# Performance work log

Hardware: AMD Instinct MI355X
Metric: run time of the kernel (lower is better)

## Reference

```python
import jax, jax.numpy as jnp
import numpy as np

D = 512      # d_encoder
H = 8        # num_attn_heads
DH = 64      # d_attn
B = 8
S = 1024


def setup_inputs() -> dict:
    key = jax.random.key(0)
    ks = jax.random.split(key, 12)
    lim_in = 1.0 / np.sqrt(D)
    inp = {
        "Q": jax.random.normal(ks[0], (B, S, D), dtype=jnp.float32),
        "K": jax.random.normal(ks[1], (B, S, D), dtype=jnp.float32),
        "V": jax.random.normal(ks[2], (B, S, D), dtype=jnp.float32),
        # per-head projection weights stacked over heads: [H, D, DH]
        "Wq": jax.random.uniform(ks[3], (H, D, DH), jnp.float32, -lim_in, lim_in),
        "bq": jax.random.uniform(ks[4], (H, DH), jnp.float32, -lim_in, lim_in),
        "Wk": jax.random.uniform(ks[5], (H, D, DH), jnp.float32, -lim_in, lim_in),
        "bk": jax.random.uniform(ks[6], (H, DH), jnp.float32, -lim_in, lim_in),
        "Wv": jax.random.uniform(ks[7], (H, D, DH), jnp.float32, -lim_in, lim_in),
        "bv": jax.random.uniform(ks[8], (H, DH), jnp.float32, -lim_in, lim_in),
        "Wo": jax.random.uniform(ks[9], (D, D), jnp.float32, -lim_in, lim_in),
        "bo": jax.random.uniform(ks[10], (D,), jnp.float32, -lim_in, lim_in),
    }
    return inp


def reference(Q, K, V, Wq, bq, Wk, bk, Wv, bv, Wo, bo):
    scale = 1.0 / np.sqrt(DH).astype(np.float32)
    # per-head projections (the torch loop over heads, batched): [B,H,S,DH]
    Qh = jnp.einsum("bsd,hde->bhse", Q, Wq) + bq[None, :, None, :]
    Kh = jnp.einsum("bsd,hde->bhse", K, Wk) + bk[None, :, None, :]
    Vh = jnp.einsum("bsd,hde->bhse", V, Wv) + bv[None, :, None, :]
    # scaled dot-product attention with materialized scores [B,H,S,S]
    scores = jnp.einsum("bhse,bhte->bhst", Qh, Kh) * scale
    probs = jax.nn.softmax(scores, axis=-1)
    x = jnp.einsum("bhst,bhte->bhse", probs, Vh)  # [B,H,S,DH]
    # NOTE: original torch code does x.view(B, S, H*DH) directly on the
    # (B,H,S,DH) contiguous tensor WITHOUT transposing heads/time; we
    # faithfully replicate that memory-layout reshape.
    x = x.reshape(B, S, H * DH)
    x = x @ Wo + bo
    # dropout p=0.0 (p_drop set to 0 for deterministic reference)
    return x
```

## Files before the change

kernel.cpp:

```cpp
#include <hip/hip_runtime.h>
#include <hip/hip_bf16.h>

#define D_ENC 512
#define NH 8
#define DHD 64
#define BB 8
#define SS 1024

typedef unsigned short u16;
typedef __attribute__((ext_vector_type(8))) short short8;
typedef __attribute__((ext_vector_type(4))) float floatx4;

#define QSCALE 0.18033688011112042f

__device__ inline u16 f2bf(float f) {
    __hip_bfloat16 h = __float2bfloat16(f);
    return *reinterpret_cast<u16*>(&h);
}

__device__ inline void glds16(const u16* g, u16* l) {
    __builtin_amdgcn_global_load_lds(
        (const __attribute__((address_space(1))) void*)g,
        (__attribute__((address_space(3))) void*)l, 16, 0, 0);
}

__global__ __launch_bounds__(256) void prep_all(
    const float* __restrict__ Wq, const float* __restrict__ Wk,
    const float* __restrict__ Wv, const float* __restrict__ Wo,
    const float* __restrict__ Q, const float* __restrict__ K,
    const float* __restrict__ V,
    u16* __restrict__ WqT, u16* __restrict__ WkT, u16* __restrict__ WvT,
    u16* __restrict__ WoT, u16* __restrict__ Xbf)
{
    int bx = blockIdx.x;
    if (bx < 4096) {
        int tid = bx * 256 + threadIdx.x;
        const int WSZ = NH * D_ENC * DHD;
        if (tid < 3 * WSZ) {
            int wi = tid / WSZ, r = tid % WSZ;
            int d = r & 511;
            int e = (r >> 9) & 63;
            int h = r >> 15;
            const float* src = wi == 0 ? Wq : (wi == 1 ? Wk : Wv);
            u16* dst = wi == 0 ? WqT : (wi == 1 ? WkT : WvT);
            dst[r] = f2bf(src[h * (D_ENC * DHD) + d * DHD + e]);
        } else {
            int r = tid - 3 * WSZ;
            int d = r & 511, n = r >> 9;
            WoT[r] = f2bf(Wo[d * D_ENC + n]);
        }
    } else {
        int t = (bx - 4096) * 256 + threadIdx.x;
        int p = t / 524288, i = t % 524288;
        const float* src = p == 0 ? Q : (p == 1 ? K : V);
        const float4* s4 = reinterpret_cast<const float4*>(src) + (size_t)i * 2;
        float4 a = s4[0], b = s4[1];
        u16 hv[8] = { f2bf(a.x), f2bf(a.y), f2bf(a.z), f2bf(a.w),
                      f2bf(b.x), f2bf(b.y), f2bf(b.z), f2bf(b.w) };
        *reinterpret_cast<uint4*>(Xbf + (size_t)t * 8) =
            *reinterpret_cast<const uint4*>(hv);
    }
}

__global__ __launch_bounds__(256, 4) void qkv_gemm(
    const u16* __restrict__ Xbf,
    const u16* __restrict__ WqT, const u16* __restrict__ WkT,
    const u16* __restrict__ WvT,
    const float* __restrict__ bq, const float* __restrict__ bk,
    const float* __restrict__ bv,
    u16* __restrict__ Qh, u16* __restrict__ Kh, u16* __restrict__ VhT)
{
    const int proj = blockIdx.z;
    const u16* X = Xbf + (size_t)proj * (BB * SS * D_ENC);
    const u16* WT = proj == 0 ? WqT : (proj == 1 ? WkT : WvT);
    const float* bias = proj == 0 ? bq : (proj == 1 ? bk : bv);
    u16* out = proj == 0 ? Qh : (proj == 1 ? Kh : VhT);
    const float oscale = proj == 0 ? QSCALE : 1.0f;

    const int m0 = blockIdx.x * 128;
    const int n0 = blockIdx.y * 64;
    __shared__ __align__(16) char smem[(128 * 64 + 64 * 64) * 2];
    u16* As = (u16*)smem;
    u16* Bs = As + 128 * 64;
    u16* Ts = (u16*)smem;

    const int tid = threadIdx.x, lane = tid & 63, w = tid >> 6;
    const int q = lane >> 4, l15 = lane & 15;
    const int lr = lane >> 3;
    const int lc = (lane & 7) ^ (lr & 7);

    floatx4 acc[2][4] = {};

    for (int d0 = 0; d0 < D_ENC; d0 += 64) {
        #pragma unroll
        for (int j = 0; j < 4; ++j) {
            int r = (j * 4 + w) * 8 + lr;
            glds16(X + (size_t)(m0 + r) * D_ENC + d0 + lc * 8,
                   As + (j * 4 + w) * 512);
        }
        #pragma unroll
        for (int j = 0; j < 2; ++j) {
            int r = (j * 4 + w) * 8 + lr;
            glds16(WT + (size_t)(n0 + r) * D_ENC + d0 + lc * 8,
                   Bs + (j * 4 + w) * 512);
        }
        __syncthreads();
        #pragma unroll
        for (int ks = 0; ks < 2; ++ks) {
            const int co = ((ks * 4 + q) ^ (l15 & 7)) * 8;
            short8 a0 = *(const short8*)&As[(32 * w + l15) * 64 + co];
            short8 a1 = *(const short8*)&As[(32 * w + 16 + l15) * 64 + co];
            #pragma unroll
            for (int f = 0; f < 4; ++f) {
                short8 bf = *(const short8*)&Bs[(f * 16 + l15) * 64 + co];
                acc[0][f] = __builtin_amdgcn_mfma_f32_16x16x32_bf16(a0, bf, acc[0][f], 0, 0, 0);
                acc[1][f] = __builtin_amdgcn_mfma_f32_16x16x32_bf16(a1, bf, acc[1][f], 0, 0, 0);
            }
        }
        __syncthreads();
    }

    const int b = m0 >> 10, sb = m0 & 1023, h = n0 >> 6;
    if (proj < 2) {
        u16* dst = out + ((size_t)(b * NH + h) * SS + sb) * DHD;
        #pragma unroll
        for (int i = 0; i < 2; ++i)
            #pragma unroll
            for (int f = 0; f < 4; ++f) {
                float bv_ = bias[n0 + f * 16 + l15];
                #pragma unroll
                for (int r = 0; r < 4; ++r)
                    dst[(32 * w + 16 * i + q * 4 + r) * DHD + f * 16 + l15] =
                        f2bf((acc[i][f][r] + bv_) * oscale);
            }
    } else {
        #pragma unroll
        for (int i = 0; i < 2; ++i)
            #pragma unroll
            for (int f = 0; f < 4; ++f) {
                float bv_ = bias[n0 + f * 16 + l15];
                #pragma unroll
                for (int r = 0; r < 4; ++r)
                    Ts[(f * 16 + l15) * 136 + 32 * w + 16 * i + q * 4 + r] =
                        f2bf(acc[i][f][r] + bv_);
            }
        __syncthreads();
        u16* dst = out + (size_t)(b * NH + h) * DHD * SS + sb;
        #pragma unroll
        for (int p2 = 0; p2 < 4; ++p2) {
            int c = (tid + 256 * p2) * 8;
            int e = c >> 7, s = c & 127;
            uint4 v = *(const uint4*)&Ts[e * 136 + s];
            *(uint4*)&dst[(size_t)e * SS + s] = v;
        }
    }
}

__global__ __launch_bounds__(256, 4) void flash_attn(
    const u16* __restrict__ Qh, const u16* __restrict__ Kh,
    const u16* __restrict__ VhT, u16* __restrict__ Xb)
{
    const int i = blockIdx.x;
    const int s0 = (i >> 6) * 64;
    const int bh_i = ((i >> 3) & 7) * 8 + (i & 7);
    const size_t bh = (size_t)bh_i;

    __shared__ __align__(16) u16 Ks[2][64 * 64], Vs[2][64 * 64], Ps[64 * 64];

    const int tid = threadIdx.x, lane = tid & 63, w = tid >> 6;
    const int q = lane >> 4, l15 = lane & 15;
    const int lr = lane >> 3, lc = (lane & 7) ^ (lr & 7);

    const u16* qrow = Qh + (bh * SS + s0 + 16 * w + l15) * DHD;
    short8 qb0 = *(const short8*)(qrow + q * 8);
    short8 qb1 = *(const short8*)(qrow + 32 + q * 8);

    const u16* kbase = Kh + bh * SS * DHD;
    const u16* vbase = VhT + bh * DHD * SS;

    #pragma unroll
    for (int j = 0; j < 2; ++j) {
        int r = (j * 4 + w) * 8 + lr;
        glds16(kbase + (size_t)r * DHD + lc * 8, Ks[0] + (j * 4 + w) * 512);
        glds16(vbase + (size_t)r * SS + lc * 8, Vs[0] + (j * 4 + w) * 512);
    }

    floatx4 O[4] = {};
    floatx4 L = {0.f, 0.f, 0.f, 0.f};
    const short8 ones = {16256, 16256, 16256, 16256,
                         16256, 16256, 16256, 16256};

    for (int kt = 0; kt < SS / 64; ++kt) {
        __syncthreads();
        if (kt + 1 < SS / 64) {
            const int k1 = (kt + 1) * 64;
            u16* kd = Ks[(kt + 1) & 1];
            u16* vd = Vs[(kt + 1) & 1];
            #pragma unroll
            for (int j = 0; j < 2; ++j) {
                int r = (j * 4 + w) * 8 + lr;
                glds16(kbase + (size_t)(k1 + r) * DHD + lc * 8,
                       kd + (j * 4 + w) * 512);
                glds16(vbase + (size_t)r * SS + k1 + lc * 8,
                       vd + (j * 4 + w) * 512);
            }
        }
        const u16* ks_ = Ks[kt & 1];
        const u16* vs_ = Vs[kt & 1];

        floatx4 sacc[4] = {};
        #pragma unroll
        for (int f = 0; f < 4; ++f) {
            const int co0 = (q ^ (l15 & 7)) * 8;
            const int co1 = ((4 + q) ^ (l15 & 7)) * 8;
            short8 ka0 = *(const short8*)&ks_[(f * 16 + l15) * 64 + co0];
            short8 ka1 = *(const short8*)&ks_[(f * 16 + l15) * 64 + co1];
            sacc[f] = __builtin_amdgcn_mfma_f32_16x16x32_bf16(ka0, qb0, sacc[f], 0, 0, 0);
            sacc[f] = __builtin_amdgcn_mfma_f32_16x16x32_bf16(ka1, qb1, sacc[f], 0, 0, 0);
        }

        #pragma unroll
        for (int f = 0; f < 4; ++f) {
            ushort4 pk;
            pk.x = f2bf(__builtin_amdgcn_exp2f(sacc[f][0]));
            pk.y = f2bf(__builtin_amdgcn_exp2f(sacc[f][1]));
            pk.z = f2bf(__builtin_amdgcn_exp2f(sacc[f][2]));
            pk.w = f2bf(__builtin_amdgcn_exp2f(sacc[f][3]));
            const int chunk = (2 * f + (q >> 1)) ^ (l15 & 7);
            *(ushort4*)&Ps[(16 * w + l15) * 64 + chunk * 8 + (q & 1) * 4] = pk;
        }

        #pragma unroll
        for (int ks = 0; ks < 2; ++ks) {
            const int co = ((ks * 4 + q) ^ (l15 & 7)) * 8;
            short8 pa = *(const short8*)&Ps[(16 * w + l15) * 64 + co];
            L = __builtin_amdgcn_mfma_f32_16x16x32_bf16(pa, ones, L, 0, 0, 0);
            #pragma unroll
            for (int f = 0; f < 4; ++f) {
                short8 vb = *(const short8*)&vs_[(f * 16 + l15) * 64 + co];
                O[f] = __builtin_amdgcn_mfma_f32_16x16x32_bf16(pa, vb, O[f], 0, 0, 0);
            }
        }
    }

    u16* dst = Xb + (bh * SS + s0) * DHD;
    #pragma unroll
    for (int f = 0; f < 4; ++f)
        #pragma unroll
        for (int r = 0; r < 4; ++r)
            dst[(16 * w + q * 4 + r) * DHD + f * 16 + l15] =
                f2bf(O[f][r] / L[r]);
}

__global__ __launch_bounds__(256, 4) void out_gemm(
    const u16* __restrict__ X, const u16* __restrict__ WT,
    const float* __restrict__ bias, float* __restrict__ out)
{
    const int m0 = blockIdx.x * 128;
    const int n0 = blockIdx.y * 64;
    __shared__ __align__(16) u16 As[128 * 64];
    __shared__ __align__(16) u16 Bs[64 * 64];

    const int tid = threadIdx.x, lane = tid & 63, w = tid >> 6;
    const int q = lane >> 4, l15 = lane & 15;
    const int lr = lane >> 3, lc = (lane & 7) ^ (lr & 7);

    floatx4 acc[2][4] = {};

    for (int d0 = 0; d0 < D_ENC; d0 += 64) {
        #pragma unroll
        for (int j = 0; j < 4; ++j) {
            int r = (j * 4 + w) * 8 + lr;
            glds16(X + (size_t)(m0 + r) * D_ENC + d0 + lc * 8,
                   As + (j * 4 + w) * 512);
        }
        #pragma unroll
        for (int j = 0; j < 2; ++j) {
            int r = (j * 4 + w) * 8 + lr;
            glds16(WT + (size_t)(n0 + r) * D_ENC + d0 + lc * 8,
                   Bs + (j * 4 + w) * 512);
        }
        __syncthreads();
        #pragma unroll
        for (int ks = 0; ks < 2; ++ks) {
            const int co = ((ks * 4 + q) ^ (l15 & 7)) * 8;
            short8 a0 = *(const short8*)&As[(32 * w + l15) * 64 + co];
            short8 a1 = *(const short8*)&As[(32 * w + 16 + l15) * 64 + co];
            #pragma unroll
            for (int f = 0; f < 4; ++f) {
                short8 bf = *(const short8*)&Bs[(f * 16 + l15) * 64 + co];
                acc[0][f] = __builtin_amdgcn_mfma_f32_16x16x32_bf16(a0, bf, acc[0][f], 0, 0, 0);
                acc[1][f] = __builtin_amdgcn_mfma_f32_16x16x32_bf16(a1, bf, acc[1][f], 0, 0, 0);
            }
        }
        __syncthreads();
    }
    #pragma unroll
    for (int i = 0; i < 2; ++i)
        #pragma unroll
        for (int f = 0; f < 4; ++f) {
            float bv_ = bias[n0 + f * 16 + l15];
            #pragma unroll
            for (int r = 0; r < 4; ++r)
                out[(size_t)(m0 + 32 * w + 16 * i + q * 4 + r) * D_ENC +
                    n0 + f * 16 + l15] = acc[i][f][r] + bv_;
        }
}

extern "C" void kernel_launch(void* const* d_in, const int* in_sizes, int n_in,
                              void* d_out, int out_size, void* d_ws, size_t ws_size,
                              hipStream_t stream)
{
    const float* Q  = (const float*)d_in[0];
    const float* K  = (const float*)d_in[1];
    const float* V  = (const float*)d_in[2];
    const float* Wq = (const float*)d_in[3];
    const float* bq = (const float*)d_in[4];
    const float* Wk = (const float*)d_in[5];
    const float* bk = (const float*)d_in[6];
    const float* Wv = (const float*)d_in[7];
    const float* bv = (const float*)d_in[8];
    const float* Wo = (const float*)d_in[9];
    const float* bo = (const float*)d_in[10];
    float* out = (float*)d_out;

    char* ws = (char*)d_ws;
    u16* WqT = (u16*)(ws + 0);
    u16* WkT = (u16*)(ws + 524288);
    u16* WvT = (u16*)(ws + 1048576);
    u16* WoT = (u16*)(ws + 1572864);
    u16* Xbf = (u16*)(ws + 2097152);
    u16* Xb  = (u16*)(ws + 2097152);
    u16* Qh  = (u16*)(ws + 27262976);
    u16* Kh  = (u16*)(ws + 35651584);
    u16* VhT = (u16*)(ws + 44040192);

    hipLaunchKernelGGL(prep_all, dim3(10240), dim3(256), 0, stream,
                       Wq, Wk, Wv, Wo, Q, K, V, WqT, WkT, WvT, WoT, Xbf);
    hipLaunchKernelGGL(qkv_gemm, dim3(64, 8, 3), dim3(256), 0, stream,
                       Xbf, WqT, WkT, WvT, bq, bk, bv, Qh, Kh, VhT);
    hipLaunchKernelGGL(flash_attn, dim3(1024), dim3(256), 0, stream,
                       Qh, Kh, VhT, Xb);
    hipLaunchKernelGGL(out_gemm, dim3(64, 8), dim3(256), 0, stream,
                       Xb, WoT, bo, out);
}
```

Before: 165.9 us.

## Process 128 query rows per flash-attention block to double K/V tile reuse

Result: slower. 172.4 us (+3.9%).

```diff
diff --git a/kernel.cpp b/kernel.cpp
--- a/kernel.cpp
+++ b/kernel.cpp
@@ -156,14 +156,13 @@
     }
 }
 
-__global__ __launch_bounds__(256, 4) void flash_attn(
+__global__ __launch_bounds__(256, 2) void flash_attn(
     const u16* __restrict__ Qh, const u16* __restrict__ Kh,
     const u16* __restrict__ VhT, u16* __restrict__ Xb)
 {
     const int i = blockIdx.x;
-    const int s0 = (i >> 6) * 64;
-    const int bh_i = ((i >> 3) & 7) * 8 + (i & 7);
-    const size_t bh = (size_t)bh_i;
+    const int s0 = (i >> 6) * 128;
+    const size_t bh = (size_t)(((i >> 3) & 7) * 8 + (i & 7));
 
     __shared__ __align__(16) u16 Ks[2][64 * 64], Vs[2][64 * 64], Ps[64 * 64];
 
@@ -171,9 +170,13 @@
     const int q = lane >> 4, l15 = lane & 15;
     const int lr = lane >> 3, lc = (lane & 7) ^ (lr & 7);
 
-    const u16* qrow = Qh + (bh * SS + s0 + 16 * w + l15) * DHD;
-    short8 qb0 = *(const short8*)(qrow + q * 8);
-    short8 qb1 = *(const short8*)(qrow + 32 + q * 8);
+    short8 qb[2][2];
+    #pragma unroll
+    for (int g = 0; g < 2; ++g) {
+        const u16* qrow = Qh + (bh * SS + s0 + 32 * w + 16 * g + l15) * DHD;
+        qb[g][0] = *(const short8*)(qrow + q * 8);
+        qb[g][1] = *(const short8*)(qrow + 32 + q * 8);
+    }
 
     const u16* kbase = Kh + bh * SS * DHD;
     const u16* vbase = VhT + bh * DHD * SS;
@@ -185,8 +188,8 @@
         glds16(vbase + (size_t)r * SS + lc * 8, Vs[0] + (j * 4 + w) * 512);
     }
 
-    floatx4 O[4] = {};
-    floatx4 L = {0.f, 0.f, 0.f, 0.f};
+    floatx4 O[2][4] = {};
+    floatx4 L[2] = {};
     const short8 ones = {16256, 16256, 16256, 16256,
                          16256, 16256, 16256, 16256};
 
@@ -208,48 +211,54 @@
         const u16* ks_ = Ks[kt & 1];
         const u16* vs_ = Vs[kt & 1];
 
-        floatx4 sacc[4] = {};
-        #pragma unroll
-        for (int f = 0; f < 4; ++f) {
-            const int co0 = (q ^ (l15 & 7)) * 8;
-            const int co1 = ((4 + q) ^ (l15 & 7)) * 8;
-            short8 ka0 = *(const short8*)&ks_[(f * 16 + l15) * 64 + co0];
-            short8 ka1 = *(const short8*)&ks_[(f * 16 + l15) * 64 + co1];
-            sacc[f] = __builtin_amdgcn_mfma_f32_16x16x32_bf16(ka0, qb0, sacc[f], 0, 0, 0);
-            sacc[f] = __builtin_amdgcn_mfma_f32_16x16x32_bf16(ka1, qb1, sacc[f], 0, 0, 0);
-        }
-
-        #pragma unroll
-        for (int f = 0; f < 4; ++f) {
-            ushort4 pk;
-            pk.x = f2bf(__builtin_amdgcn_exp2f(sacc[f][0]));
-            pk.y = f2bf(__builtin_amdgcn_exp2f(sacc[f][1]));
-            pk.z = f2bf(__builtin_amdgcn_exp2f(sacc[f][2]));
-            pk.w = f2bf(__builtin_amdgcn_exp2f(sacc[f][3]));
-            const int chunk = (2 * f + (q >> 1)) ^ (l15 & 7);
-            *(ushort4*)&Ps[(16 * w + l15) * 64 + chunk * 8 + (q & 1) * 4] = pk;
-        }
-
-        #pragma unroll
-        for (int ks = 0; ks < 2; ++ks) {
-            const int co = ((ks * 4 + q) ^ (l15 & 7)) * 8;
-            short8 pa = *(const short8*)&Ps[(16 * w + l15) * 64 + co];
-            L = __builtin_amdgcn_mfma_f32_16x16x32_bf16(pa, ones, L, 0, 0, 0);
-            #pragma unroll
-            for (int f = 0; f < 4; ++f) {
-                short8 vb = *(const short8*)&vs_[(f * 16 + l15) * 64 + co];
-                O[f] = __builtin_amdgcn_mfma_f32_16x16x32_bf16(pa, vb, O[f], 0, 0, 0);
-            }
-        }
-    }
-
-    u16* dst = Xb + (bh * SS + s0) * DHD;
+        #pragma unroll
+        for (int g = 0; g < 2; ++g) {
+            floatx4 sacc[4] = {};
+            #pragma unroll
+            for (int f = 0; f < 4; ++f) {
+                const int co0 = (q ^ (l15 & 7)) * 8;
+                const int co1 = ((4 + q) ^ (l15 & 7)) * 8;
+                short8 ka0 = *(const short8*)&ks_[(f * 16 + l15) * 64 + co0];
+                short8 ka1 = *(const short8*)&ks_[(f * 16 + l15) * 64 + co1];
+                sacc[f] = __builtin_amdgcn_mfma_f32_16x16x32_bf16(ka0, qb[g][0], sacc[f], 0, 0, 0);
+                sacc[f] = __builtin_amdgcn_mfma_f32_16x16x32_bf16(ka1, qb[g][1], sacc[f], 0, 0, 0);
+            }
+
+            #pragma unroll
+            for (int f = 0; f < 4; ++f) {
+                ushort4 pk;
+                pk.x = f2bf(__builtin_amdgcn_exp2f(sacc[f][0]));
+                pk.y = f2bf(__builtin_amdgcn_exp2f(sacc[f][1]));
+                pk.z = f2bf(__builtin_amdgcn_exp2f(sacc[f][2]));
+                pk.w = f2bf(__builtin_amdgcn_exp2f(sacc[f][3]));
+                const int chunk = (2 * f + (q >> 1)) ^ (l15 & 7);
+                *(ushort4*)&Ps[(16 * w + l15) * 64 + chunk * 8 + (q & 1) * 4] = pk;
+            }
+
+            #pragma unroll
+            for (int ks = 0; ks < 2; ++ks) {
+                const int co = ((ks * 4 + q) ^ (l15 & 7)) * 8;
+                short8 pa = *(const short8*)&Ps[(16 * w + l15) * 64 + co];
+                L[g] = __builtin_amdgcn_mfma_f32_16x16x32_bf16(pa, ones, L[g], 0, 0, 0);
+                #pragma unroll
+                for (int f = 0; f < 4; ++f) {
+                    short8 vb = *(const short8*)&vs_[(f * 16 + l15) * 64 + co];
+                    O[g][f] = __builtin_amdgcn_mfma_f32_16x16x32_bf16(pa, vb, O[g][f], 0, 0, 0);
+                }
+            }
+        }
+    }
+
     #pragma unroll
-    for (int f = 0; f < 4; ++f)
-        #pragma unroll
-        for (int r = 0; r < 4; ++r)
-            dst[(16 * w + q * 4 + r) * DHD + f * 16 + l15] =
-                f2bf(O[f][r] / L[r]);
+    for (int g = 0; g < 2; ++g) {
+        u16* dst = Xb + (bh * SS + s0 + 32 * w + 16 * g) * DHD;
+        #pragma unroll
+        for (int f = 0; f < 4; ++f)
+            #pragma unroll
+            for (int r = 0; r < 4; ++r)
+                dst[(q * 4 + r) * DHD + f * 16 + l15] =
+                    f2bf(O[g][f][r] / L[g][r]);
+    }
 }
 
 __global__ __launch_bounds__(256, 4) void out_gemm(
@@ -339,7 +348,7 @@
                        Wq, Wk, Wv, Wo, Q, K, V, WqT, WkT, WvT, WoT, Xbf);
     hipLaunchKernelGGL(qkv_gemm, dim3(64, 8, 3), dim3(256), 0, stream,
                        Xbf, WqT, WkT, WvT, bq, bk, bv, Qh, Kh, VhT);
-    hipLaunchKernelGGL(flash_attn, dim3(1024), dim3(256), 0, stream,
+    hipLaunchKernelGGL(flash_attn, dim3(512), dim3(256), 0, stream,
                        Qh, Kh, VhT, Xb);
     hipLaunchKernelGGL(out_gemm, dim3(64, 8), dim3(256), 0, stream,
                        Xb, WoT, bo, out);
```
